# Kernel optimization log

Hardware: AMD Instinct MI355X
Metric: run time of the kernel (lower is better)

## Reference

```python
import jax, jax.numpy as jnp
import numpy as np

N_NODES = 50000
N_EDGES = 800000
H_NODE = 128
H_EDGE = 128
EPS = 1e-5


def _bn(x, gamma, beta):
    # training-mode BatchNorm1d over axis 0 (biased variance)
    mean = jnp.mean(x, axis=0)
    var = jnp.var(x, axis=0)
    return (x - mean) * jax.lax.rsqrt(var + EPS) * gamma + beta


def setup_inputs() -> dict:
    key = jax.random.key(0)
    ks = jax.random.split(key, 8)
    d_in = H_NODE + H_EDGE          # 256
    d_out = 2 * H_NODE              # 256
    bound = 1.0 / np.sqrt(d_in)
    return {
        "node_emb": jax.random.normal(ks[0], (N_NODES, H_NODE), jnp.float32),
        "edge_emb": jax.random.normal(ks[1], (N_EDGES, H_EDGE), jnp.float32),
        "i": jax.random.randint(ks[2], (N_EDGES,), 0, N_NODES, jnp.int64),
        "w1": jax.random.uniform(ks[3], (d_out, d_in), jnp.float32, -bound, bound),
        "b1": jax.random.uniform(ks[4], (d_out,), jnp.float32, -bound, bound),
        "g1": jnp.ones((d_out,), jnp.float32),
        "be1": jnp.zeros((d_out,), jnp.float32),
        "g2": jnp.ones((H_NODE,), jnp.float32),
        "be2": jnp.zeros((H_NODE,), jnp.float32),
    }


def reference(node_emb, edge_emb, i, w1, b1, g1, be1, g2, be2):
    # gather + concat: [E, H_NODE + H_EDGE]
    c1 = jnp.concatenate([node_emb[i], edge_emb], axis=1)
    # linear -> BN: [E, 2*H_NODE]
    c1 = _bn(c1 @ w1.T + b1, g1, be1)
    c1_filter, c1_core = jnp.split(c1, 2, axis=1)
    msg = jax.nn.sigmoid(c1_filter) * jnp.tanh(c1_core)  # [E, H_NODE]
    # scatter-sum back to nodes
    c1_emb = jax.ops.segment_sum(msg, i, num_segments=node_emb.shape[0])
    c1_emb = _bn(c1_emb, g2, be2)
    return jnp.tanh(node_emb + c1_emb)
```

## Files before the change

kernel.cpp:

```cpp
#include <hip/hip_runtime.h>
#include <hip/hip_fp16.h>
#include <cstdint>
#include <cstddef>

#define NN 50000
#define NE 800000
#define EPSV 1e-5f
#define NTILES (NE / 128)
#define PGRID 1024

typedef _Float16 f16_t;
typedef f16_t f16x8 __attribute__((ext_vector_type(8)));
typedef f16_t f16x4 __attribute__((ext_vector_type(4)));
typedef f16_t f16x2 __attribute__((ext_vector_type(2)));
typedef float f32x4 __attribute__((ext_vector_type(4)));

__device__ __forceinline__ float fast_tanh(float x) {
  float e2 = __expf(2.f * x);
  return 1.f - 2.f / (e2 + 1.f);
}
__device__ __forceinline__ float fast_sigmoid(float x) {
  return 1.f / (1.f + __expf(-x));
}

__launch_bounds__(256, 4)
__global__ void node_proj(const float* __restrict__ A, const float* __restrict__ w1,
                          const float* __restrict__ b1, f16_t* __restrict__ P) {
  __shared__ f16_t Alds[128][136];
  const int tid = threadIdx.x;
  const int wave = tid >> 6;
  const int lane = tid & 63;
  const int quad = lane >> 4;
  const int l16 = lane & 15;

  int cols[4];
#pragma unroll
  for (int nt = 0; nt < 4; ++nt) cols[nt] = 16 * wave + 64 * nt + l16;

  f16x8 bfrag[4][4];
#pragma unroll
  for (int nt = 0; nt < 4; ++nt)
#pragma unroll
    for (int ks = 0; ks < 4; ++ks) {
      const float* src = w1 + (size_t)cols[nt] * 256 + ks * 32 + quad * 8;
#pragma unroll
      for (int j = 0; j < 8; ++j) bfrag[nt][ks][j] = (f16_t)src[j];
    }

  float c0[4];
#pragma unroll
  for (int nt = 0; nt < 4; ++nt) c0[nt] = b1[cols[nt]];

  const int row0 = blockIdx.x * 128;
  {
    const int r = tid >> 1, half = tid & 1;
    const int grow = row0 + r;
    f16_t* dst = &Alds[r][half * 64];
    if (grow < NN) {
      const float4* src = (const float4*)(A + (size_t)grow * 128 + half * 64);
#pragma unroll
      for (int c = 0; c < 8; ++c) {
        float4 v0 = src[2 * c], v1 = src[2 * c + 1];
        f16x8 pk = {(f16_t)v0.x, (f16_t)v0.y, (f16_t)v0.z, (f16_t)v0.w,
                    (f16_t)v1.x, (f16_t)v1.y, (f16_t)v1.z, (f16_t)v1.w};
        *(f16x8*)(dst + c * 8) = pk;
      }
    } else {
      f16x8 z = {0, 0, 0, 0, 0, 0, 0, 0};
#pragma unroll
      for (int c = 0; c < 8; ++c) *(f16x8*)(dst + c * 8) = z;
    }
  }
  __syncthreads();

#pragma unroll 1
  for (int m = 0; m < 8; ++m) {
    f16x8 afrag[4];
#pragma unroll
    for (int ks = 0; ks < 4; ++ks)
      afrag[ks] = *(const f16x8*)&Alds[m * 16 + l16][ks * 32 + quad * 8];
    f32x4 acc[4];
#pragma unroll
    for (int nt = 0; nt < 4; ++nt) acc[nt] = (f32x4){0.f, 0.f, 0.f, 0.f};
#pragma unroll
    for (int ks = 0; ks < 4; ++ks)
#pragma unroll
      for (int nt = 0; nt < 4; ++nt)
        acc[nt] = __builtin_amdgcn_mfma_f32_16x16x32_f16(
            afrag[ks], bfrag[nt][ks], acc[nt], 0, 0, 0);
    const int rbase = row0 + m * 16 + quad * 4;
#pragma unroll
    for (int reg = 0; reg < 4; ++reg) {
      int g = rbase + reg;
      if (g < NN) {
        f16x4 pk;
#pragma unroll
        for (int nt = 0; nt < 4; ++nt) pk[nt] = (f16_t)(acc[nt][reg] + c0[nt]);
        *(f16x4*)&P[(size_t)g * 256 + wave * 64 + l16 * 4] = pk;
      }
    }
  }
}

template <int MODE>
__launch_bounds__(256, 4)
__global__ void edge_pass(const float* __restrict__ A, const float* __restrict__ w1,
                          const int* __restrict__ idx, const f16_t* __restrict__ P,
                          float* __restrict__ stats, const float* __restrict__ st,
                          f16_t* __restrict__ acc16, int* __restrict__ ctr) {
  __shared__ f16_t Alds[128][136];
  __shared__ int sIdx[128];
  __shared__ int s_tile;
  const int tid = threadIdx.x;
  const int wave = tid >> 6;
  const int lane = tid & 63;
  const int quad = lane >> 4;
  const int l16 = lane & 15;

  int cols[4];
#pragma unroll
  for (int nt = 0; nt < 4; ++nt) cols[nt] = 16 * wave + 64 * nt + l16;

  f16x8 bfrag[4][4];
#pragma unroll
  for (int nt = 0; nt < 4; ++nt)
#pragma unroll
    for (int ks = 0; ks < 4; ++ks) {
      const float* src = w1 + (size_t)cols[nt] * 256 + 128 + ks * 32 + quad * 8;
#pragma unroll
      for (int j = 0; j < 8; ++j) bfrag[nt][ks][j] = (f16_t)src[j];
    }

  float c0[4], c1c[4];
  if (MODE == 2) {
#pragma unroll
    for (int nt = 0; nt < 4; ++nt) {
      c0[nt] = st[cols[nt]];
      c1c[nt] = st[256 + cols[nt]];
    }
  }
  float ssum[4] = {0.f, 0.f, 0.f, 0.f};
  float ssq[4] = {0.f, 0.f, 0.f, 0.f};

  for (;;) {
    if (tid == 0) s_tile = atomicAdd(ctr, 1);
    __syncthreads();
    const int t = s_tile;
    if (t >= NTILES) break;
    const int row0 = t * 128;

    if (tid < 128) sIdx[tid] = idx[row0 + tid];
    {
      const int r = tid >> 1, half = tid & 1;
      const float4* src = (const float4*)(A + (size_t)(row0 + r) * 128 + half * 64);
      f16_t* dst = &Alds[r][half * 64];
#pragma unroll
      for (int c = 0; c < 8; ++c) {
        float4 v0 = src[2 * c], v1 = src[2 * c + 1];
        f16x8 pk = {(f16_t)v0.x, (f16_t)v0.y, (f16_t)v0.z, (f16_t)v0.w,
                    (f16_t)v1.x, (f16_t)v1.y, (f16_t)v1.z, (f16_t)v1.w};
        *(f16x8*)(dst + c * 8) = pk;
      }
    }
    __syncthreads();

#pragma unroll 1
    for (int m = 0; m < 8; ++m) {
      f16x8 afrag[4];
#pragma unroll
      for (int ks = 0; ks < 4; ++ks)
        afrag[ks] = *(const f16x8*)&Alds[m * 16 + l16][ks * 32 + quad * 8];

      int node[4];
      f16x4 pv[4];
#pragma unroll
      for (int reg = 0; reg < 4; ++reg) {
        node[reg] = sIdx[m * 16 + quad * 4 + reg];
        pv[reg] = *(const f16x4*)&P[(size_t)node[reg] * 256 + wave * 64 + l16 * 4];
      }

      f32x4 acc[4];
#pragma unroll
      for (int nt = 0; nt < 4; ++nt) acc[nt] = (f32x4){0.f, 0.f, 0.f, 0.f};
#pragma unroll
      for (int ks = 0; ks < 4; ++ks)
#pragma unroll
        for (int nt = 0; nt < 4; ++nt)
          acc[nt] = __builtin_amdgcn_mfma_f32_16x16x32_f16(
              afrag[ks], bfrag[nt][ks], acc[nt], 0, 0, 0);

#pragma unroll
      for (int reg = 0; reg < 4; ++reg) {
        float h[4];
#pragma unroll
        for (int nt = 0; nt < 4; ++nt) h[nt] = acc[nt][reg] + (float)pv[reg][nt];
        if (MODE == 2) {
          float hn[4];
#pragma unroll
          for (int nt = 0; nt < 4; ++nt) hn[nt] = h[nt] * c0[nt] + c1c[nt];
          float msg0 = fast_sigmoid(hn[0]) * fast_tanh(hn[2]);
          float msg1 = fast_sigmoid(hn[1]) * fast_tanh(hn[3]);
          float o0 = __shfl_xor(msg0, 1);
          float o1 = __shfl_xor(msg1, 1);
          const bool ev = (l16 & 1) == 0;
          f16x2 val;
          val[0] = (f16_t)(ev ? msg0 : o1);
          val[1] = (f16_t)(ev ? o0 : msg1);
          const int colb = 16 * wave + (ev ? 0 : 64) + (l16 & ~1);
          __half2* addr = (__half2*)&acc16[(size_t)node[reg] * 128 + colb];
          unsafeAtomicAdd(addr, *(__half2*)&val);
        } else {
#pragma unroll
          for (int nt = 0; nt < 4; ++nt) {
            ssum[nt] += h[nt];
            ssq[nt] += h[nt] * h[nt];
          }
          if (MODE == 3) {
            f16x4 hp;
#pragma unroll
            for (int nt = 0; nt < 4; ++nt) hp[nt] = (f16_t)h[nt];
            const int edge = row0 + m * 16 + quad * 4 + reg;
            *(f16x4*)&acc16[(size_t)edge * 256 + wave * 64 + l16 * 4] = hp;
          }
        }
      }
    }
    __syncthreads();
  }

  if (MODE == 1 || MODE == 3) {
#pragma unroll
    for (int nt = 0; nt < 4; ++nt) {
      float s = ssum[nt], q = ssq[nt];
      s += __shfl_xor(s, 16); s += __shfl_xor(s, 32);
      q += __shfl_xor(q, 16); q += __shfl_xor(q, 32);
      if (quad == 0) {
        atomicAdd(&stats[cols[nt]], s);
        atomicAdd(&stats[256 + cols[nt]], q);
      }
    }
  }
}

__global__ void finalize1(const float* __restrict__ stats, const float* __restrict__ g1,
                          const float* __restrict__ be1, float* __restrict__ st,
                          float* __restrict__ st_sw) {
  int j = threadIdx.x;
  float mean = stats[j] * (1.f / NE);
  float var = stats[256 + j] * (1.f / NE) - mean * mean;
  float s = g1[j] * rsqrtf(var + EPSV);
  float t = be1[j] - mean * s;
  st[j] = s;
  st[256 + j] = t;
  int w = (j & 63) >> 4, nt = j >> 6, l16 = j & 15;
  int p = w * 64 + l16 * 4 + nt;
  st_sw[p] = s;
  st_sw[256 + p] = t;
}

__launch_bounds__(256, 8)
__global__ void edge_apply(const f16_t* __restrict__ hsw, const int* __restrict__ idx,
                           const float* __restrict__ stw, f16_t* __restrict__ acc16) {
  const int i = blockIdx.x * 256 + threadIdx.x;
  const int e = i >> 5;
  const int k2 = i & 31;
  const int node = idx[e];
  const f16x8 h8 = *(const f16x8*)&hsw[(size_t)e * 256 + k2 * 8];
  const float4* sv = (const float4*)stw;
  const float4 s0 = sv[2 * k2], s1 = sv[2 * k2 + 1];
  const float4 t0 = sv[64 + 2 * k2], t1 = sv[64 + 2 * k2 + 1];
  const float hn0 = (float)h8[0] * s0.x + t0.x;
  const float hn1 = (float)h8[1] * s0.y + t0.y;
  const float hn2 = (float)h8[2] * s0.z + t0.z;
  const float hn3 = (float)h8[3] * s0.w + t0.w;
  const float hn4 = (float)h8[4] * s1.x + t1.x;
  const float hn5 = (float)h8[5] * s1.y + t1.y;
  const float hn6 = (float)h8[6] * s1.z + t1.z;
  const float hn7 = (float)h8[7] * s1.w + t1.w;
  f16x2 va, vb;
  va[0] = (f16_t)(fast_sigmoid(hn0) * fast_tanh(hn2));
  va[1] = (f16_t)(fast_sigmoid(hn4) * fast_tanh(hn6));
  vb[0] = (f16_t)(fast_sigmoid(hn1) * fast_tanh(hn3));
  vb[1] = (f16_t)(fast_sigmoid(hn5) * fast_tanh(hn7));
  f16_t* rowp = acc16 + (size_t)node * 128;
  const int cA = 16 * (k2 >> 3) + ((k2 & 7) << 1);
  unsafeAtomicAdd((__half2*)(rowp + cA), *(__half2*)&va);
  unsafeAtomicAdd((__half2*)(rowp + 64 + cA), *(__half2*)&vb);
}

__global__ void bn2_stats(const f16_t* __restrict__ acc16, float* __restrict__ stats) {
  const int tid = threadIdx.x;
  const int c2 = tid & 63;
  const int ph = tid >> 6;
  float s0 = 0.f, s1 = 0.f, q0 = 0.f, q1 = 0.f;
  for (int row = blockIdx.x * 4 + ph; row < NN; row += gridDim.x * 4) {
    f16x2 v = *(const f16x2*)&acc16[(size_t)row * 128 + 2 * c2];
    float a = (float)v[0], b = (float)v[1];
    s0 += a; q0 += a * a;
    s1 += b; q1 += b * b;
  }
  __shared__ float red[256][4];
  red[tid][0] = s0; red[tid][1] = s1; red[tid][2] = q0; red[tid][3] = q1;
  __syncthreads();
  if (ph == 0) {
    float a0 = 0.f, a1 = 0.f, b0 = 0.f, b1 = 0.f;
#pragma unroll
    for (int p = 0; p < 4; ++p) {
      a0 += red[p * 64 + c2][0]; a1 += red[p * 64 + c2][1];
      b0 += red[p * 64 + c2][2]; b1 += red[p * 64 + c2][3];
    }
    atomicAdd(&stats[2 * c2], a0);
    atomicAdd(&stats[2 * c2 + 1], a1);
    atomicAdd(&stats[128 + 2 * c2], b0);
    atomicAdd(&stats[128 + 2 * c2 + 1], b1);
  }
}

__global__ void finalize2(const float* __restrict__ stats, const float* __restrict__ g2,
                          const float* __restrict__ be2, float* __restrict__ sc) {
  int j = threadIdx.x;
  float mean = stats[j] * (1.f / NN);
  float var = stats[128 + j] * (1.f / NN) - mean * mean;
  float s = g2[j] * rsqrtf(var + EPSV);
  sc[j] = s;
  sc[128 + j] = be2[j] - mean * s;
}

__global__ void final_kernel(const float* __restrict__ node_emb, const float* __restrict__ sc,
                             const f16_t* __restrict__ acc16, float* __restrict__ out) {
  int i = blockIdx.x * blockDim.x + threadIdx.x;
  if (i >= NN * 32) return;
  int c4 = i & 31;
  int row = i >> 5;
  float4 s4 = ((const float4*)sc)[c4];
  float4 h4 = ((const float4*)(sc + 128))[c4];
  float4 ne = ((const float4*)node_emb)[i];
  f16x4 cv = *(const f16x4*)&acc16[(size_t)row * 128 + c4 * 4];
  float4 r;
  r.x = fast_tanh(ne.x + (float)cv[0] * s4.x + h4.x);
  r.y = fast_tanh(ne.y + (float)cv[1] * s4.y + h4.y);
  r.z = fast_tanh(ne.z + (float)cv[2] * s4.z + h4.z);
  r.w = fast_tanh(ne.w + (float)cv[3] * s4.w + h4.w);
  ((float4*)out)[i] = r;
}

extern "C" void kernel_launch(void* const* d_in, const int* in_sizes, int n_in,
                              void* d_out, int out_size, void* d_ws, size_t ws_size,
                              hipStream_t stream) {
  (void)in_sizes; (void)n_in; (void)out_size;
  const float* node_emb = (const float*)d_in[0];
  const float* edge_emb = (const float*)d_in[1];
  const int* idx = (const int*)d_in[2];
  const float* w1 = (const float*)d_in[3];
  const float* b1 = (const float*)d_in[4];
  const float* g1 = (const float*)d_in[5];
  const float* be1 = (const float*)d_in[6];
  const float* g2 = (const float*)d_in[7];
  const float* be2 = (const float*)d_in[8];
  float* out = (float*)d_out;

  float* wsf = (float*)d_ws;
  float* bn1sums = wsf;
  float* st = wsf + 512;
  float* bn2sums = wsf + 1024;
  float* sc2 = wsf + 1280;
  int* ctr1 = (int*)(wsf + 1536);
  int* ctr2 = (int*)(wsf + 1537);
  float* st_sw = wsf + 2048;
  char* base = (char*)d_ws + 16384;
  f16_t* P = (f16_t*)base;
  f16_t* acc16 = (f16_t*)(base + (size_t)NN * 512);
  f16_t* hsw = (f16_t*)(base + (size_t)NN * 512 + (size_t)NN * 256);
  const size_t need = 16384 + (size_t)NN * 512 + (size_t)NN * 256 + (size_t)NE * 512;

  hipMemsetAsync(wsf, 0, 2048 * sizeof(float), stream);
  hipMemsetAsync(acc16, 0, (size_t)NN * 256, stream);

  node_proj<<<(NN + 127) / 128, 256, 0, stream>>>(node_emb, w1, b1, P);
  if (ws_size >= need) {
    edge_pass<3><<<PGRID, 256, 0, stream>>>(edge_emb, w1, idx, P, bn1sums, nullptr,
                                            hsw, ctr1);
    finalize1<<<1, 256, 0, stream>>>(bn1sums, g1, be1, st, st_sw);
    edge_apply<<<NE * 32 / 256, 256, 0, stream>>>(hsw, idx, st_sw, acc16);
  } else {
    edge_pass<1><<<PGRID, 256, 0, stream>>>(edge_emb, w1, idx, P, bn1sums, nullptr,
                                            nullptr, ctr1);
    finalize1<<<1, 256, 0, stream>>>(bn1sums, g1, be1, st, st_sw);
    edge_pass<2><<<PGRID, 256, 0, stream>>>(edge_emb, w1, idx, P, nullptr, st,
                                            acc16, ctr2);
  }
  bn2_stats<<<128, 256, 0, stream>>>(acc16, bn2sums);
  finalize2<<<1, 128, 0, stream>>>(bn2sums, g2, be2, sc2);
  final_kernel<<<(NN * 32 + 255) / 256, 256, 0, stream>>>(node_emb, sc2, acc16, out);
}
```

Measured before the change: 901.8 us.

## Replace atomic scatter with CSR-sorted gather for segment sum

Builds a CSR edge list per destination node (count, single-block scan, atomic fill) each call, then a new gather_apply kernel has each half-wave accumulate all incoming edges of a node in fp32 registers and write the row once. This removes the f16 atomic adds into acc16 and the memset of acc16. The cost is three extra kernels, an 800K-entry index array, and random row gathers of hsw in place of streaming reads. Whether it runs depends on the workspace being large enough for the extra CSR buffers.

```diff
diff --git a/kernel.cpp b/kernel.cpp
--- a/kernel.cpp
+++ b/kernel.cpp
@@ -8,6 +8,8 @@
 #define EPSV 1e-5f
 #define NTILES (NE / 128)
 #define PGRID 1024
+#define SCAN_T 1024
+#define CHUNK ((NN + SCAN_T - 1) / SCAN_T)
 
 typedef _Float16 f16_t;
 typedef f16_t f16x8 __attribute__((ext_vector_type(8)));
@@ -258,6 +260,115 @@
   st_sw[256 + p] = t;
 }
 
+__global__ void csr_count(const int* __restrict__ idx, int* __restrict__ cnt) {
+  int i = blockIdx.x * 256 + threadIdx.x;
+  if (i < NE / 4) {
+    int4 v = ((const int4*)idx)[i];
+    atomicAdd(&cnt[v.x], 1);
+    atomicAdd(&cnt[v.y], 1);
+    atomicAdd(&cnt[v.z], 1);
+    atomicAdd(&cnt[v.w], 1);
+  }
+}
+
+__global__ void csr_scan(const int* __restrict__ cnt, int* __restrict__ off,
+                         int* __restrict__ cur) {
+  __shared__ int ls[SCAN_T];
+  const int t = threadIdx.x;
+  const int b0 = t * CHUNK;
+  int s = 0;
+  for (int k = 0; k < CHUNK; ++k) {
+    int n = b0 + k;
+    if (n < NN) s += cnt[n];
+  }
+  ls[t] = s;
+  __syncthreads();
+  for (int d = 1; d < SCAN_T; d <<= 1) {
+    int u = (t >= d) ? ls[t - d] : 0;
+    __syncthreads();
+    ls[t] += u;
+    __syncthreads();
+  }
+  int run = ls[t] - s;
+  for (int k = 0; k < CHUNK; ++k) {
+    int n = b0 + k;
+    if (n < NN) {
+      off[n] = run;
+      cur[n] = run;
+      run += cnt[n];
+    }
+  }
+  if (t == SCAN_T - 1) off[NN] = run;
+}
+
+__global__ void csr_fill(const int* __restrict__ idx, int* __restrict__ cur,
+                         int* __restrict__ elist) {
+  int i = blockIdx.x * 256 + threadIdx.x;
+  if (i < NE / 4) {
+    int4 v = ((const int4*)idx)[i];
+    int e = 4 * i;
+    elist[atomicAdd(&cur[v.x], 1)] = e;
+    elist[atomicAdd(&cur[v.y], 1)] = e + 1;
+    elist[atomicAdd(&cur[v.z], 1)] = e + 2;
+    elist[atomicAdd(&cur[v.w], 1)] = e + 3;
+  }
+}
+
+__device__ __forceinline__ void acc_edge(const f16x8 h, const float4 sA,
+                                         const float4 sB, const float4 tA,
+                                         const float4 tB, float& a0, float& a1,
+                                         float& b0, float& b1) {
+  a0 += fast_sigmoid((float)h[0] * sA.x + tA.x) * fast_tanh((float)h[2] * sA.z + tA.z);
+  b0 += fast_sigmoid((float)h[1] * sA.y + tA.y) * fast_tanh((float)h[3] * sA.w + tA.w);
+  a1 += fast_sigmoid((float)h[4] * sB.x + tB.x) * fast_tanh((float)h[6] * sB.z + tB.z);
+  b1 += fast_sigmoid((float)h[5] * sB.y + tB.y) * fast_tanh((float)h[7] * sB.w + tB.w);
+}
+
+__launch_bounds__(256, 8)
+__global__ void gather_apply(const f16_t* __restrict__ hsw, const int* __restrict__ off,
+                             const int* __restrict__ elist, const float* __restrict__ stw,
+                             f16_t* __restrict__ acc16, int* __restrict__ ctr) {
+  const int tid = threadIdx.x;
+  const int lane = tid & 63;
+  const int k2 = tid & 31;
+  const float4 sA = *(const float4*)&stw[8 * k2];
+  const float4 sB = *(const float4*)&stw[8 * k2 + 4];
+  const float4 tA = *(const float4*)&stw[256 + 8 * k2];
+  const float4 tB = *(const float4*)&stw[256 + 8 * k2 + 4];
+  const int cA = 16 * (k2 >> 3) + ((k2 & 7) << 1);
+
+  for (;;) {
+    int nb = 0;
+    if (k2 == 0) nb = atomicAdd(ctr, 1);
+    nb = __shfl(nb, lane & 32);
+    const int n0 = nb * 4;
+    if (n0 >= NN) break;
+    const int n1 = (n0 + 4 < NN) ? n0 + 4 : NN;
+    for (int n = n0; n < n1; ++n) {
+      const int s = off[n], e = off[n + 1];
+      float a0 = 0.f, a1 = 0.f, b0 = 0.f, b1 = 0.f;
+      int j = s;
+      for (; j + 2 <= e; j += 2) {
+        const int e0 = elist[j], e1 = elist[j + 1];
+        const f16x8 h0 = *(const f16x8*)&hsw[(size_t)e0 * 256 + k2 * 8];
+        const f16x8 h1 = *(const f16x8*)&hsw[(size_t)e1 * 256 + k2 * 8];
+        acc_edge(h0, sA, sB, tA, tB, a0, a1, b0, b1);
+        acc_edge(h1, sA, sB, tA, tB, a0, a1, b0, b1);
+      }
+      if (j < e) {
+        const int e0 = elist[j];
+        const f16x8 h0 = *(const f16x8*)&hsw[(size_t)e0 * 256 + k2 * 8];
+        acc_edge(h0, sA, sB, tA, tB, a0, a1, b0, b1);
+      }
+      f16x2 va, vb;
+      va[0] = (f16_t)a0; va[1] = (f16_t)a1;
+      vb[0] = (f16_t)b0; vb[1] = (f16_t)b1;
+      *(f16x2*)&acc16[(size_t)n * 128 + cA] = va;
+      *(f16x2*)&acc16[(size_t)n * 128 + 64 + cA] = vb;
+    }
+  }
+}
+
 __launch_bounds__(256, 8)
 __global__ void edge_apply(const f16_t* __restrict__ hsw, const int* __restrict__ idx,
                            const float* __restrict__ stw, f16_t* __restrict__ acc16) {
@@ -266,24 +377,21 @@
   const int k2 = i & 31;
   const int node = idx[e];
   const f16x8 h8 = *(const f16x8*)&hsw[(size_t)e * 256 + k2 * 8];
-  const float4* sv = (const float4*)stw;
-  const float4 s0 = sv[2 * k2], s1 = sv[2 * k2 + 1];
-  const float4 t0 = sv[64 + 2 * k2], t1 = sv[64 + 2 * k2 + 1];
-  const float hn0 = (float)h8[0] * s0.x + t0.x;
-  const float hn1 = (float)h8[1] * s0.y + t0.y;
-  const float hn2 = (float)h8[2] * s0.z + t0.z;
-  const float hn3 = (float)h8[3] * s0.w + t0.w;
-  const float hn4 = (float)h8[4] * s1.x + t1.x;
-  const float hn5 = (float)h8[5] * s1.y + t1.y;
-  const float hn6 = (float)h8[6] * s1.z + t1.z;
-  const float hn7 = (float)h8[7] * s1.w + t1.w;
+  const float4 sA = *(const float4*)&stw[8 * k2];
+  const float4 sB = *(const float4*)&stw[8 * k2 + 4];
+  const float4 tA = *(const float4*)&stw[256 + 8 * k2];
+  const float4 tB = *(const float4*)&stw[256 + 8 * k2 + 4];
   f16x2 va, vb;
-  va[0] = (f16_t)(fast_sigmoid(hn0) * fast_tanh(hn2));
-  va[1] = (f16_t)(fast_sigmoid(hn4) * fast_tanh(hn6));
-  vb[0] = (f16_t)(fast_sigmoid(hn1) * fast_tanh(hn3));
-  vb[1] = (f16_t)(fast_sigmoid(hn5) * fast_tanh(hn7));
+  va[0] = (f16_t)(fast_sigmoid((float)h8[0] * sA.x + tA.x) *
+                  fast_tanh((float)h8[2] * sA.z + tA.z));
+  va[1] = (f16_t)(fast_sigmoid((float)h8[4] * sB.x + tB.x) *
+                  fast_tanh((float)h8[6] * sB.z + tB.z));
+  vb[0] = (f16_t)(fast_sigmoid((float)h8[1] * sA.y + tA.y) *
+                  fast_tanh((float)h8[3] * sA.w + tA.w));
+  vb[1] = (f16_t)(fast_sigmoid((float)h8[5] * sB.y + tB.y) *
+                  fast_tanh((float)h8[7] * sB.w + tB.w));
+  const int cA = 16 * (k2 >> 3) + ((k2 & 7) << 1);
   f16_t* rowp = acc16 + (size_t)node * 128;
-  const int cA = 16 * (k2 >> 3) + ((k2 & 7) << 1);
   unsafeAtomicAdd((__half2*)(rowp + cA), *(__half2*)&va);
   unsafeAtomicAdd((__half2*)(rowp + 64 + cA), *(__half2*)&vb);
 }
@@ -371,18 +479,34 @@
   f16_t* P = (f16_t*)base;
   f16_t* acc16 = (f16_t*)(base + (size_t)NN * 512);
   f16_t* hsw = (f16_t*)(base + (size_t)NN * 512 + (size_t)NN * 256);
-  const size_t need = 16384 + (size_t)NN * 512 + (size_t)NN * 256 + (size_t)NE * 512;
+  int* cnt = (int*)(base + (size_t)NN * 512 + (size_t)NN * 256 + (size_t)NE * 512);
+  int* off = cnt + NN;
+  int* cur = off + NN + 1;
+  int* elist = cur + NN;
+
+  const size_t need_r1 = 16384 + (size_t)NN * 512 + (size_t)NN * 256 + (size_t)NE * 512;
+  const size_t need_full = need_r1 + sizeof(int) * (size_t)(3 * NN + 1 + NE);
 
   hipMemsetAsync(wsf, 0, 2048 * sizeof(float), stream);
-  hipMemsetAsync(acc16, 0, (size_t)NN * 256, stream);
 
   node_proj<<<(NN + 127) / 128, 256, 0, stream>>>(node_emb, w1, b1, P);
-  if (ws_size >= need) {
+  if (ws_size >= need_full) {
+    hipMemsetAsync(cnt, 0, sizeof(int) * NN, stream);
+    csr_count<<<(NE / 4 + 255) / 256, 256, 0, stream>>>(idx, cnt);
+    csr_scan<<<1, SCAN_T, 0, stream>>>(cnt, off, cur);
+    csr_fill<<<(NE / 4 + 255) / 256, 256, 0, stream>>>(idx, cur, elist);
+    edge_pass<3><<<PGRID, 256, 0, stream>>>(edge_emb, w1, idx, P, bn1sums, nullptr,
+                                            hsw, ctr1);
+    finalize1<<<1, 256, 0, stream>>>(bn1sums, g1, be1, st, st_sw);
+    gather_apply<<<2048, 256, 0, stream>>>(hsw, off, elist, st_sw, acc16, ctr2);
+  } else if (ws_size >= need_r1) {
+    hipMemsetAsync(acc16, 0, (size_t)NN * 256, stream);
     edge_pass<3><<<PGRID, 256, 0, stream>>>(edge_emb, w1, idx, P, bn1sums, nullptr,
                                             hsw, ctr1);
     finalize1<<<1, 256, 0, stream>>>(bn1sums, g1, be1, st, st_sw);
     edge_apply<<<NE * 32 / 256, 256, 0, stream>>>(hsw, idx, st_sw, acc16);
   } else {
+    hipMemsetAsync(acc16, 0, (size_t)NN * 256, stream);
     edge_pass<1><<<PGRID, 256, 0, stream>>>(edge_emb, w1, idx, P, bn1sums, nullptr,
                                             nullptr, ctr1);
     finalize1<<<1, 256, 0, stream>>>(bn1sums, g1, be1, st, st_sw);
```

Measured after the change: 1.215 ms. +34.7%, slower.

## Split edge GEMM across 8 waves, fold finalize2 into final kernel

Applied to the files above, without the earlier changes.

The edge pass now runs 512-thread blocks with 8 waves, each owning 2 output column tiles instead of 4. This halves per-wave B fragments and accumulators and changes the P and hsw layouts to paired columns, with matching updates in node_proj, finalize1 and edge_apply. Separately, the finalize2 launch is removed by having every thread of final_kernel recompute the BN2 scale and shift from the raw sums, and bn2_stats gets more blocks. The aim is higher occupancy and fewer launches, at the cost of redundant per-thread rsqrt work and narrower gather loads.

```diff
diff --git a/kernel.cpp b/kernel.cpp
--- a/kernel.cpp
+++ b/kernel.cpp
@@ -7,7 +7,7 @@
 #define NE 800000
 #define EPSV 1e-5f
 #define NTILES (NE / 128)
-#define PGRID 1024
+#define EGRID 768
 
 typedef _Float16 f16_t;
 typedef f16_t f16x8 __attribute__((ext_vector_type(8)));
@@ -93,54 +93,57 @@
     for (int reg = 0; reg < 4; ++reg) {
       int g = rbase + reg;
       if (g < NN) {
-        f16x4 pk;
-#pragma unroll
-        for (int nt = 0; nt < 4; ++nt) pk[nt] = (f16_t)(acc[nt][reg] + c0[nt]);
-        *(f16x4*)&P[(size_t)g * 256 + wave * 64 + l16 * 4] = pk;
+        f16x2 pA, pB;
+        pA[0] = (f16_t)(acc[0][reg] + c0[0]);
+        pA[1] = (f16_t)(acc[2][reg] + c0[2]);
+        pB[0] = (f16_t)(acc[1][reg] + c0[1]);
+        pB[1] = (f16_t)(acc[3][reg] + c0[3]);
+        *(f16x2*)&P[(size_t)g * 256 + wave * 32 + l16 * 2] = pA;
+        *(f16x2*)&P[(size_t)g * 256 + (wave + 4) * 32 + l16 * 2] = pB;
       }
     }
   }
 }
 
 template <int MODE>
-__launch_bounds__(256, 4)
+__launch_bounds__(512, 6)
 __global__ void edge_pass(const float* __restrict__ A, const float* __restrict__ w1,
                           const int* __restrict__ idx, const f16_t* __restrict__ P,
                           float* __restrict__ stats, const float* __restrict__ st,
-                          f16_t* __restrict__ acc16, int* __restrict__ ctr) {
+                          f16_t* __restrict__ outp, int* __restrict__ ctr) {
   __shared__ f16_t Alds[128][136];
   __shared__ int sIdx[128];
   __shared__ int s_tile;
   const int tid = threadIdx.x;
-  const int wave = tid >> 6;
+  const int w = tid >> 6;
   const int lane = tid & 63;
   const int quad = lane >> 4;
   const int l16 = lane & 15;
 
-  int cols[4];
-#pragma unroll
-  for (int nt = 0; nt < 4; ++nt) cols[nt] = 16 * wave + 64 * nt + l16;
-
-  f16x8 bfrag[4][4];
-#pragma unroll
-  for (int nt = 0; nt < 4; ++nt)
+  int cols[2];
+#pragma unroll
+  for (int n = 0; n < 2; ++n) cols[n] = 16 * w + 128 * n + l16;
+
+  f16x8 bfrag[2][4];
+#pragma unroll
+  for (int n = 0; n < 2; ++n)
 #pragma unroll
     for (int ks = 0; ks < 4; ++ks) {
-      const float* src = w1 + (size_t)cols[nt] * 256 + 128 + ks * 32 + quad * 8;
-#pragma unroll
-      for (int j = 0; j < 8; ++j) bfrag[nt][ks][j] = (f16_t)src[j];
-    }
-
-  float c0[4], c1c[4];
+      const float* src = w1 + (size_t)cols[n] * 256 + 128 + ks * 32 + quad * 8;
+#pragma unroll
+      for (int j = 0; j < 8; ++j) bfrag[n][ks][j] = (f16_t)src[j];
+    }
+
+  float c0[2], c1c[2];
   if (MODE == 2) {
 #pragma unroll
-    for (int nt = 0; nt < 4; ++nt) {
-      c0[nt] = st[cols[nt]];
-      c1c[nt] = st[256 + cols[nt]];
-    }
-  }
-  float ssum[4] = {0.f, 0.f, 0.f, 0.f};
-  float ssq[4] = {0.f, 0.f, 0.f, 0.f};
+    for (int n = 0; n < 2; ++n) {
+      c0[n] = st[cols[n]];
+      c1c[n] = st[256 + cols[n]];
+    }
+  }
+  float ssum[2] = {0.f, 0.f};
+  float ssq[2] = {0.f, 0.f};
 
   for (;;) {
     if (tid == 0) s_tile = atomicAdd(ctr, 1);
@@ -151,11 +154,11 @@
 
     if (tid < 128) sIdx[tid] = idx[row0 + tid];
     {
-      const int r = tid >> 1, half = tid & 1;
-      const float4* src = (const float4*)(A + (size_t)(row0 + r) * 128 + half * 64);
-      f16_t* dst = &Alds[r][half * 64];
-#pragma unroll
-      for (int c = 0; c < 8; ++c) {
+      const int r = tid >> 2, q4 = tid & 3;
+      const float4* src = (const float4*)(A + (size_t)(row0 + r) * 128 + q4 * 32);
+      f16_t* dst = &Alds[r][q4 * 32];
+#pragma unroll
+      for (int c = 0; c < 4; ++c) {
         float4 v0 = src[2 * c], v1 = src[2 * c + 1];
         f16x8 pk = {(f16_t)v0.x, (f16_t)v0.y, (f16_t)v0.z, (f16_t)v0.w,
                     (f16_t)v1.x, (f16_t)v1.y, (f16_t)v1.z, (f16_t)v1.w};
@@ -166,61 +169,54 @@
 
 #pragma unroll 1
     for (int m = 0; m < 8; ++m) {
+      int node[4];
+      f16x2 pv[4];
+#pragma unroll
+      for (int reg = 0; reg < 4; ++reg) {
+        node[reg] = sIdx[m * 16 + quad * 4 + reg];
+        pv[reg] = *(const f16x2*)&P[(size_t)node[reg] * 256 + w * 32 + l16 * 2];
+      }
+
       f16x8 afrag[4];
 #pragma unroll
       for (int ks = 0; ks < 4; ++ks)
         afrag[ks] = *(const f16x8*)&Alds[m * 16 + l16][ks * 32 + quad * 8];
 
-      int node[4];
-      f16x4 pv[4];
+      f32x4 acc[2];
+      acc[0] = (f32x4){0.f, 0.f, 0.f, 0.f};
+      acc[1] = (f32x4){0.f, 0.f, 0.f, 0.f};
+#pragma unroll
+      for (int ks = 0; ks < 4; ++ks) {
+        acc[0] = __builtin_amdgcn_mfma_f32_16x16x32_f16(afrag[ks], bfrag[0][ks],
+                                                        acc[0], 0, 0, 0);
+        acc[1] = __builtin_amdgcn_mfma_f32_16x16x32_f16(afrag[ks], bfrag[1][ks],
+                                                        acc[1], 0, 0, 0);
+      }
+
 #pragma unroll
       for (int reg = 0; reg < 4; ++reg) {
-        node[reg] = sIdx[m * 16 + quad * 4 + reg];
-        pv[reg] = *(const f16x4*)&P[(size_t)node[reg] * 256 + wave * 64 + l16 * 4];
-      }
-
-      f32x4 acc[4];
-#pragma unroll
-      for (int nt = 0; nt < 4; ++nt) acc[nt] = (f32x4){0.f, 0.f, 0.f, 0.f};
-#pragma unroll
-      for (int ks = 0; ks < 4; ++ks)
-#pragma unroll
-        for (int nt = 0; nt < 4; ++nt)
-          acc[nt] = __builtin_amdgcn_mfma_f32_16x16x32_f16(
-              afrag[ks], bfrag[nt][ks], acc[nt], 0, 0, 0);
-
-#pragma unroll
-      for (int reg = 0; reg < 4; ++reg) {
-        float h[4];
-#pragma unroll
-        for (int nt = 0; nt < 4; ++nt) h[nt] = acc[nt][reg] + (float)pv[reg][nt];
+        const float h0 = acc[0][reg] + (float)pv[reg][0];
+        const float h1 = acc[1][reg] + (float)pv[reg][1];
         if (MODE == 2) {
-          float hn[4];
-#pragma unroll
-          for (int nt = 0; nt < 4; ++nt) hn[nt] = h[nt] * c0[nt] + c1c[nt];
-          float msg0 = fast_sigmoid(hn[0]) * fast_tanh(hn[2]);
-          float msg1 = fast_sigmoid(hn[1]) * fast_tanh(hn[3]);
-          float o0 = __shfl_xor(msg0, 1);
-          float o1 = __shfl_xor(msg1, 1);
-          const bool ev = (l16 & 1) == 0;
-          f16x2 val;
-          val[0] = (f16_t)(ev ? msg0 : o1);
-          val[1] = (f16_t)(ev ? o0 : msg1);
-          const int colb = 16 * wave + (ev ? 0 : 64) + (l16 & ~1);
-          __half2* addr = (__half2*)&acc16[(size_t)node[reg] * 128 + colb];
-          unsafeAtomicAdd(addr, *(__half2*)&val);
+          const float hn0 = h0 * c0[0] + c1c[0];
+          const float hn1 = h1 * c0[1] + c1c[1];
+          const float msg = fast_sigmoid(hn0) * fast_tanh(hn1);
+          const float o = __shfl_xor(msg, 1);
+          if ((l16 & 1) == 0) {
+            f16x2 val;
+            val[0] = (f16_t)msg;
+            val[1] = (f16_t)o;
+            __half2* addr =
+                (__half2*)&outp[(size_t)node[reg] * 128 + 16 * w + (l16 & ~1)];
+            unsafeAtomicAdd(addr, *(__half2*)&val);
+          }
         } else {
-#pragma unroll
-          for (int nt = 0; nt < 4; ++nt) {
-            ssum[nt] += h[nt];
-            ssq[nt] += h[nt] * h[nt];
-          }
+          ssum[0] += h0; ssq[0] += h0 * h0;
+          ssum[1] += h1; ssq[1] += h1 * h1;
           if (MODE == 3) {
-            f16x4 hp;
-#pragma unroll
-            for (int nt = 0; nt < 4; ++nt) hp[nt] = (f16_t)h[nt];
+            f16x2 hp = {(f16_t)h0, (f16_t)h1};
             const int edge = row0 + m * 16 + quad * 4 + reg;
-            *(f16x4*)&acc16[(size_t)edge * 256 + wave * 64 + l16 * 4] = hp;
+            *(f16x2*)&outp[(size_t)edge * 256 + w * 32 + l16 * 2] = hp;
           }
         }
       }
@@ -228,15 +224,15 @@
     __syncthreads();
   }
 
-  if (MODE == 1 || MODE == 3) {
-#pragma unroll
-    for (int nt = 0; nt < 4; ++nt) {
-      float s = ssum[nt], q = ssq[nt];
+  if (MODE != 2) {
+#pragma unroll
+    for (int n = 0; n < 2; ++n) {
+      float s = ssum[n], q = ssq[n];
       s += __shfl_xor(s, 16); s += __shfl_xor(s, 32);
       q += __shfl_xor(q, 16); q += __shfl_xor(q, 32);
       if (quad == 0) {
-        atomicAdd(&stats[cols[nt]], s);
-        atomicAdd(&stats[256 + cols[nt]], q);
+        atomicAdd(&stats[cols[n]], s);
+        atomicAdd(&stats[256 + cols[n]], q);
       }
     }
   }
@@ -252,10 +248,10 @@
   float t = be1[j] - mean * s;
   st[j] = s;
   st[256 + j] = t;
-  int w = (j & 63) >> 4, nt = j >> 6, l16 = j & 15;
-  int p = w * 64 + l16 * 4 + nt;
-  st_sw[p] = s;
-  st_sw[256 + p] = t;
+  int wq = (j >> 4) & 7, n = j >> 7, lj = j & 15;
+  int pos = wq * 32 + lj * 2 + n;
+  st_sw[pos] = s;
+  st_sw[256 + pos] = t;
 }
 
 __launch_bounds__(256, 8)
@@ -265,25 +261,24 @@
   const int e = i >> 5;
   const int k2 = i & 31;
   const int node = idx[e];
-  const f16x8 h8 = *(const f16x8*)&hsw[(size_t)e * 256 + k2 * 8];
-  const float4* sv = (const float4*)stw;
-  const float4 s0 = sv[2 * k2], s1 = sv[2 * k2 + 1];
-  const float4 t0 = sv[64 + 2 * k2], t1 = sv[64 + 2 * k2 + 1];
-  const float hn0 = (float)h8[0] * s0.x + t0.x;
-  const float hn1 = (float)h8[1] * s0.y + t0.y;
-  const float hn2 = (float)h8[2] * s0.z + t0.z;
-  const float hn3 = (float)h8[3] * s0.w + t0.w;
-  const float hn4 = (float)h8[4] * s1.x + t1.x;
-  const float hn5 = (float)h8[5] * s1.y + t1.y;
-  const float hn6 = (float)h8[6] * s1.z + t1.z;
-  const float hn7 = (float)h8[7] * s1.w + t1.w;
+  const int w = k2 >> 3, lp = k2 & 7;
+  const f16x4 ha = *(const f16x4*)&hsw[(size_t)e * 256 + w * 32 + lp * 4];
+  const f16x4 hb = *(const f16x4*)&hsw[(size_t)e * 256 + (w + 4) * 32 + lp * 4];
+  const float4 sA = *(const float4*)&stw[w * 32 + lp * 4];
+  const float4 sB = *(const float4*)&stw[(w + 4) * 32 + lp * 4];
+  const float4 tA = *(const float4*)&stw[256 + w * 32 + lp * 4];
+  const float4 tB = *(const float4*)&stw[256 + (w + 4) * 32 + lp * 4];
   f16x2 va, vb;
-  va[0] = (f16_t)(fast_sigmoid(hn0) * fast_tanh(hn2));
-  va[1] = (f16_t)(fast_sigmoid(hn4) * fast_tanh(hn6));
-  vb[0] = (f16_t)(fast_sigmoid(hn1) * fast_tanh(hn3));
-  vb[1] = (f16_t)(fast_sigmoid(hn5) * fast_tanh(hn7));
+  va[0] = (f16_t)(fast_sigmoid((float)ha[0] * sA.x + tA.x) *
+                  fast_tanh((float)ha[1] * sA.y + tA.y));
+  va[1] = (f16_t)(fast_sigmoid((float)ha[2] * sA.z + tA.z) *
+                  fast_tanh((float)ha[3] * sA.w + tA.w));
+  vb[0] = (f16_t)(fast_sigmoid((float)hb[0] * sB.x + tB.x) *
+                  fast_tanh((float)hb[1] * sB.y + tB.y));
+  vb[1] = (f16_t)(fast_sigmoid((float)hb[2] * sB.z + tB.z) *
+                  fast_tanh((float)hb[3] * sB.w + tB.w));
+  const int cA = 16 * w + 2 * lp;
   f16_t* rowp = acc16 + (size_t)node * 128;
-  const int cA = 16 * (k2 >> 3) + ((k2 & 7) << 1);
   unsafeAtomicAdd((__half2*)(rowp + cA), *(__half2*)&va);
   unsafeAtomicAdd((__half2*)(rowp + 64 + cA), *(__half2*)&vb);
 }
@@ -316,24 +311,30 @@
   }
 }
 
-__global__ void finalize2(const float* __restrict__ stats, const float* __restrict__ g2,
-                          const float* __restrict__ be2, float* __restrict__ sc) {
-  int j = threadIdx.x;
-  float mean = stats[j] * (1.f / NN);
-  float var = stats[128 + j] * (1.f / NN) - mean * mean;
-  float s = g2[j] * rsqrtf(var + EPSV);
-  sc[j] = s;
-  sc[128 + j] = be2[j] - mean * s;
-}
-
-__global__ void final_kernel(const float* __restrict__ node_emb, const float* __restrict__ sc,
+__global__ void final_kernel(const float* __restrict__ node_emb,
+                             const float* __restrict__ bn2sums,
+                             const float* __restrict__ g2, const float* __restrict__ be2,
                              const f16_t* __restrict__ acc16, float* __restrict__ out) {
   int i = blockIdx.x * blockDim.x + threadIdx.x;
   if (i >= NN * 32) return;
   int c4 = i & 31;
   int row = i >> 5;
-  float4 s4 = ((const float4*)sc)[c4];
-  float4 h4 = ((const float4*)(sc + 128))[c4];
+  float4 sm = ((const float4*)bn2sums)[c4];
+  float4 sq = ((const float4*)(bn2sums + 128))[c4];
+  float4 g = ((const float4*)g2)[c4];
+  float4 b = ((const float4*)be2)[c4];
+  float4 s4, h4;
+  {
+    float mean, var;
+    mean = sm.x * (1.f / NN); var = sq.x * (1.f / NN) - mean * mean;
+    s4.x = g.x * rsqrtf(var + EPSV); h4.x = b.x - mean * s4.x;
+    mean = sm.y * (1.f / NN); var = sq.y * (1.f / NN) - mean * mean;
+    s4.y = g.y * rsqrtf(var + EPSV); h4.y = b.y - mean * s4.y;
+    mean = sm.z * (1.f / NN); var = sq.z * (1.f / NN) - mean * mean;
+    s4.z = g.z * rsqrtf(var + EPSV); h4.z = b.z - mean * s4.z;
+    mean = sm.w * (1.f / NN); var = sq.w * (1.f / NN) - mean * mean;
+    s4.w = g.w * rsqrtf(var + EPSV); h4.w = b.w - mean * s4.w;
+  }
   float4 ne = ((const float4*)node_emb)[i];
   f16x4 cv = *(const f16x4*)&acc16[(size_t)row * 128 + c4 * 4];
   float4 r;
@@ -363,7 +364,6 @@
   float* bn1sums = wsf;
   float* st = wsf + 512;
   float* bn2sums = wsf + 1024;
-  float* sc2 = wsf + 1280;
   int* ctr1 = (int*)(wsf + 1536);
   int* ctr2 = (int*)(wsf + 1537);
   float* st_sw = wsf + 2048;
@@ -371,25 +371,25 @@
   f16_t* P = (f16_t*)base;
   f16_t* acc16 = (f16_t*)(base + (size_t)NN * 512);
   f16_t* hsw = (f16_t*)(base + (size_t)NN * 512 + (size_t)NN * 256);
-  const size_t need = 16384 + (size_t)NN * 512 + (size_t)NN * 256 + (size_t)NE * 512;
-
-  hipMemsetAsync(wsf, 0, 2048 * sizeof(float), stream);
+  const size_t need_h = 16384 + (size_t)NN * 512 + (size_t)NN * 256 + (size_t)NE * 512;
+
+  hipMemsetAsync(wsf, 0, 2560 * sizeof(float), stream);
   hipMemsetAsync(acc16, 0, (size_t)NN * 256, stream);
 
   node_proj<<<(NN + 127) / 128, 256, 0, stream>>>(node_emb, w1, b1, P);
-  if (ws_size >= need) {
-    edge_pass<3><<<PGRID, 256, 0, stream>>>(edge_emb, w1, idx, P, bn1sums, nullptr,
+  if (ws_size >= need_h) {
+    edge_pass<3><<<EGRID, 512, 0, stream>>>(edge_emb, w1, idx, P, bn1sums, nullptr,
                                             hsw, ctr1);
     finalize1<<<1, 256, 0, stream>>>(bn1sums, g1, be1, st, st_sw);
     edge_apply<<<NE * 32 / 256, 256, 0, stream>>>(hsw, idx, st_sw, acc16);
   } else {
-    edge_pass<1><<<PGRID, 256, 0, stream>>>(edge_emb, w1, idx, P, bn1sums, nullptr,
+    edge_pass<1><<<EGRID, 512, 0, stream>>>(edge_emb, w1, idx, P, bn1sums, nullptr,
                                             nullptr, ctr1);
     finalize1<<<1, 256, 0, stream>>>(bn1sums, g1, be1, st, st_sw);
-    edge_pass<2><<<PGRID, 256, 0, stream>>>(edge_emb, w1, idx, P, nullptr, st,
+    edge_pass<2><<<EGRID, 512, 0, stream>>>(edge_emb, w1, idx, P, bn1sums, st,
                                             acc16, ctr2);
   }
-  bn2_stats<<<128, 256, 0, stream>>>(acc16, bn2sums);
-  finalize2<<<1, 128, 0, stream>>>(bn2sums, g2, be2, sc2);
-  final_kernel<<<(NN * 32 + 255) / 256, 256, 0, stream>>>(node_emb, sc2, acc16, out);
-}
+  bn2_stats<<<256, 256, 0, stream>>>(acc16, bn2sums);
+  final_kernel<<<(NN * 32 + 255) / 256, 256, 0, stream>>>(node_emb, bn2sums, g2,
+                                                          be2, acc16, out);
+}
```

Result: no change. 900.2 us (-0.2%).
